# Kernel tuning notes

Hardware: AMD Instinct MI355X
Metric: run time of the kernel (lower is better)

## Reference

```python
import jax, jax.numpy as jnp
import numpy as np

N, IN_SIZE, FEAT, N_OUT = 8192, 512, 128, 512
ALPHA = 0.5


def setup_inputs() -> dict:
    key = jax.random.key(0)
    ks = jax.random.split(key, 5)
    return {
        "x": jax.random.normal(ks[0], (N, IN_SIZE), dtype=jnp.float32),
        "W0": jax.random.normal(ks[1], (FEAT, IN_SIZE), dtype=jnp.float32) * (1.0 / np.sqrt(IN_SIZE)),
        "W1": jax.random.normal(ks[2], (FEAT, IN_SIZE), dtype=jnp.float32) * (1.0 / np.sqrt(IN_SIZE)),
        "weight": jax.random.normal(ks[3], (IN_SIZE, N_OUT), dtype=jnp.float32),
        "weight_time": jax.random.normal(ks[4], (IN_SIZE, N_OUT), dtype=jnp.float32),
    }


def time_affinity(n: int) -> jnp.ndarray:
    # Closed form of the numpy roll/triu/flip construction: M[i,j] = n - |i-j|,
    # then rows normalized to sum to 1.
    idx = jnp.arange(n)
    M = (n - jnp.abs(idx[:, None] - idx[None, :])).astype(jnp.float32)
    return M / jnp.sum(M, axis=1, keepdims=True)


def reference(x, W0, W1, weight, weight_time):
    n = x.shape[0]
    q = x @ W0.T                      # [N, FEAT]
    k = x @ W1.T                      # [N, FEAT]
    G = jax.nn.softmax(q @ k.T, axis=1)   # [N, N] learned affinity
    G_time = time_affinity(n)              # [N, N] static affinity
    out = (G @ x) @ weight                 # [N, N_OUT]
    out_time = (G_time @ x) @ weight_time  # [N, N_OUT]
    return ALPHA * out + (1.0 - ALPHA) * out_time
```

## Files before the change

kernel.cpp:

```cpp
#include <hip/hip_runtime.h>
#include <math.h>

#define NN 8192
#define INS 512
#define FEAT 128

typedef unsigned short ush;
typedef short bf16x8 __attribute__((ext_vector_type(8)));
typedef float f32x4 __attribute__((ext_vector_type(4)));

__device__ __forceinline__ ush f2bf(float f) {
    unsigned u = __float_as_uint(f);
    unsigned r = (u + 0x7FFFu + ((u >> 16) & 1u)) >> 16;
    return (ush)r;
}
__device__ __forceinline__ float bf2f(ush h) {
    return __uint_as_float(((unsigned)h) << 16);
}
__device__ __forceinline__ void cp16(const ush* g, ush* l) {
    __builtin_amdgcn_global_load_lds(
        (const __attribute__((address_space(1))) void*)g,
        (__attribute__((address_space(3))) void*)l, 16, 0, 0);
}
__device__ __forceinline__ void split8(float4 f0, float4 f1, uint4& h, uint4& l) {
    float f[8] = {f0.x, f0.y, f0.z, f0.w, f1.x, f1.y, f1.z, f1.w};
    unsigned hu[8], lu[8];
    #pragma unroll
    for (int j = 0; j < 8; ++j) {
        unsigned u = __float_as_uint(f[j]);
        hu[j] = u >> 16;
        float lo = f[j] - __uint_as_float(u & 0xFFFF0000u);
        lu[j] = (unsigned)f2bf(lo);
    }
    h.x = hu[0] | (hu[1] << 16); h.y = hu[2] | (hu[3] << 16);
    h.z = hu[4] | (hu[5] << 16); h.w = hu[6] | (hu[7] << 16);
    l.x = lu[0] | (lu[1] << 16); l.y = lu[2] | (lu[3] << 16);
    l.z = lu[4] | (lu[5] << 16); l.w = lu[6] | (lu[7] << 16);
}


__global__ __launch_bounds__(256) void cast_w01(const float* __restrict__ W0,
                                                const float* __restrict__ W1,
                                                ush* __restrict__ W01h,
                                                ush* __restrict__ W01l) {
    int idx = (blockIdx.x * 256 + threadIdx.x) * 8;
    int r = idx >> 9, c = idx & 511;
    const float* src = (r < 128) ? &W0[r * 512 + c] : &W1[(r - 128) * 512 + c];
    float4 f0 = *(const float4*)src;
    float4 f1 = *(const float4*)(src + 4);
    uint4 h, l;
    split8(f0, f1, h, l);
    *(uint4*)&W01h[idx] = h;
    *(uint4*)&W01l[idx] = l;
}

__global__ __launch_bounds__(256) void cast_wT(const float* __restrict__ wm,
                                               const float* __restrict__ wt,
                                               ush* __restrict__ wmTh, ush* __restrict__ wmTl,
                                               ush* __restrict__ wtTh, ush* __restrict__ wtTl) {
    const float* src = blockIdx.z ? wt : wm;
    ush* oh = blockIdx.z ? wtTh : wmTh;
    ush* ol = blockIdx.z ? wtTl : wmTl;
    __shared__ float T[64][65];
    const int t = threadIdx.x;
    const int k0 = blockIdx.y * 64, n0 = blockIdx.x * 64;
    #pragma unroll
    for (int u = 0; u < 4; ++u) {
        int idx = u * 256 + t;
        int r = idx >> 4, c4 = (idx & 15) * 4;
        *(float4*)&T[r][c4] = *(const float4*)&src[(k0 + r) * 512 + n0 + c4];
    }
    __syncthreads();
    #pragma unroll
    for (int u = 0; u < 4; ++u) {
        int idx = u * 256 + t;
        int a = idx >> 4, b4 = (idx & 15) * 4;
        unsigned hu[4], lu[4];
        #pragma unroll
        for (int j = 0; j < 4; ++j) {
            float f = T[b4 + j][a];
            unsigned uu = __float_as_uint(f);
            hu[j] = uu >> 16;
            lu[j] = (unsigned)f2bf(f - __uint_as_float(uu & 0xFFFF0000u));
        }
        uint2 hp, lp;
        hp.x = hu[0] | (hu[1] << 16); hp.y = hu[2] | (hu[3] << 16);
        lp.x = lu[0] | (lu[1] << 16); lp.y = lu[2] | (lu[3] << 16);
        *(uint2*)&oh[(n0 + a) * 512 + k0 + b4] = hp;
        *(uint2*)&ol[(n0 + a) * 512 + k0 + b4] = lp;
    }
}

__global__ __launch_bounds__(256) void gemm_xv(const float* __restrict__ x,
    const ush* __restrict__ wmTh, const ush* __restrict__ wmTl,
    const ush* __restrict__ wtTh, const ush* __restrict__ wtTl,
    ush* __restrict__ vtg, ush* __restrict__ xtb) {
    const bool isV = (blockIdx.z == 0);
    const ush* Bhg = isV ? wmTh : wtTh;
    const ush* Blg = isV ? wmTl : wtTl;
    __shared__ __align__(16) ush sm[20480];
    ush* Ah = sm;
    ush* Al = sm + 5120;
    ush* Bh = sm + 10240;
    ush* Bl = sm + 15360;
    const int t = threadIdx.x;
    const int lane = t & 63, w = t >> 6;
    const int l15 = lane & 15, g4 = lane >> 4;
    const int m0 = blockIdx.y * 128, n0 = blockIdx.x * 128;
    const int wm0 = (w & 1) * 64, wn0 = (w >> 1) * 64;
    f32x4 acc[4][4];
    #pragma unroll
    for (int mt = 0; mt < 4; ++mt)
        #pragma unroll
        for (int nt = 0; nt < 4; ++nt)
            acc[mt][nt] = (f32x4){0.f, 0.f, 0.f, 0.f};

    const int am = t >> 1, akh = (t & 1) * 16;
    for (int k0 = 0; k0 < 512; k0 += 32) {
        __syncthreads();
        {
            const float* src = &x[(m0 + am) * 512 + k0 + akh];
            float4 f0 = *(const float4*)&src[0];
            float4 f1 = *(const float4*)&src[4];
            float4 f2 = *(const float4*)&src[8];
            float4 f3 = *(const float4*)&src[12];
            uint4 h0, l0, h1, l1;
            split8(f0, f1, h0, l0);
            split8(f2, f3, h1, l1);
            int s0 = am * 5 + (akh >> 3);
            *(uint4*)&Ah[s0 * 8] = h0; *(uint4*)&Ah[(s0 + 1) * 8] = h1;
            *(uint4*)&Al[s0 * 8] = l0; *(uint4*)&Al[(s0 + 1) * 8] = l1;
        }
        #pragma unroll
        for (int u = 0; u < 2; ++u) {
            int s = u * 256 + t;
            int n = s >> 2, g = s & 3;
            int srco = (n0 + n) * 512 + k0 + g * 8;
            int slot = n * 5 + g;
            *(uint4*)&Bh[slot * 8] = *(const uint4*)&Bhg[srco];
            *(uint4*)&Bl[slot * 8] = *(const uint4*)&Blg[srco];
        }
        __syncthreads();
        bf16x8 ah[4], al[4], bh[4], bl[4];
        #pragma unroll
        for (int mt = 0; mt < 4; ++mt) {
            int slot = (wm0 + mt * 16 + l15) * 5 + g4;
            ah[mt] = *(const bf16x8*)&Ah[slot * 8];
            al[mt] = *(const bf16x8*)&Al[slot * 8];
        }
        #pragma unroll
        for (int nt = 0; nt < 4; ++nt) {
            int slot = (wn0 + nt * 16 + l15) * 5 + g4;
            bh[nt] = *(const bf16x8*)&Bh[slot * 8];
            bl[nt] = *(const bf16x8*)&Bl[slot * 8];
        }
        #pragma unroll
        for (int mt = 0; mt < 4; ++mt)
            #pragma unroll
            for (int nt = 0; nt < 4; ++nt) {
                acc[mt][nt] = __builtin_amdgcn_mfma_f32_16x16x32_bf16(ah[mt], bh[nt], acc[mt][nt], 0, 0, 0);
                acc[mt][nt] = __builtin_amdgcn_mfma_f32_16x16x32_bf16(al[mt], bh[nt], acc[mt][nt], 0, 0, 0);
                acc[mt][nt] = __builtin_amdgcn_mfma_f32_16x16x32_bf16(ah[mt], bl[nt], acc[mt][nt], 0, 0, 0);
            }
    }

    if (!isV) {
        #pragma unroll
        for (int mt = 0; mt < 4; ++mt)
            #pragma unroll
            for (int nt = 0; nt < 4; ++nt) {
                int col = n0 + wn0 + nt * 16 + l15;
                int rowb = m0 + wm0 + mt * 16 + g4 * 4;
                #pragma unroll
                for (int reg = 0; reg < 4; ++reg)
                    xtb[(rowb + reg) * 512 + col] = f2bf(acc[mt][nt][reg]);
            }
    } else {
        __syncthreads();
        #pragma unroll
        for (int mt = 0; mt < 4; ++mt)
            #pragma unroll
            for (int nt = 0; nt < 4; ++nt) {
                int nl = wn0 + nt * 16 + l15;
                int mb = wm0 + mt * 16 + g4 * 4;
                uint2 pk;
                pk.x = (unsigned)f2bf(acc[mt][nt][0]) | ((unsigned)f2bf(acc[mt][nt][1]) << 16);
                pk.y = (unsigned)f2bf(acc[mt][nt][2]) | ((unsigned)f2bf(acc[mt][nt][3]) << 16);
                *(uint2*)&sm[nl * 136 + mb] = pk;
            }
        __syncthreads();
        int a = t >> 1, off = (t & 1) * 64;
        #pragma unroll
        for (int u = 0; u < 8; ++u)
            *(uint4*)&vtg[(n0 + a) * 8192 + m0 + off + u * 8] =
                *(const uint4*)&sm[a * 136 + off + u * 8];
    }
}

__global__ __launch_bounds__(256) void gemm_qk(const float* __restrict__ x,
    const ush* __restrict__ W01h, const ush* __restrict__ W01l,
    ush* __restrict__ qh, ush* __restrict__ ql,
    ush* __restrict__ kh, ush* __restrict__ kl) {
    __shared__ __align__(16) ush sm[15360];
    ush* Ah = sm;
    ush* Al = sm + 2560;
    ush* Bh = sm + 5120;
    ush* Bl = sm + 10240;
    const int t = threadIdx.x;
    const int lane = t & 63, w = t >> 6;
    const int l15 = lane & 15, g4 = lane >> 4;
    const int m0 = blockIdx.y * 64, n0 = blockIdx.x * 128;
    const int wm0 = (w & 1) * 32, wn0 = (w >> 1) * 64;
    f32x4 acc[2][4];
    #pragma unroll
    for (int mt = 0; mt < 2; ++mt)
        #pragma unroll
        for (int nt = 0; nt < 4; ++nt)
            acc[mt][nt] = (f32x4){0.f, 0.f, 0.f, 0.f};

    const int ar = t >> 2, ag = t & 3;
    for (int k0 = 0; k0 < 512; k0 += 32) {
        __syncthreads();
        {
            const float* src = &x[(m0 + ar) * 512 + k0 + ag * 8];
            float4 f0 = *(const float4*)&src[0];
            float4 f1 = *(const float4*)&src[4];
            uint4 h, l;
            split8(f0, f1, h, l);
            int slot = ar * 5 + ag;
            *(uint4*)&Ah[slot * 8] = h;
            *(uint4*)&Al[slot * 8] = l;
        }
        #pragma unroll
        for (int u = 0; u < 2; ++u) {
            int s = u * 256 + t;
            int n = s >> 2, g = s & 3;
            int srco = (n0 + n) * 512 + k0 + g * 8;
            int slot = n * 5 + g;
            *(uint4*)&Bh[slot * 8] = *(const uint4*)&W01h[srco];
            *(uint4*)&Bl[slot * 8] = *(const uint4*)&W01l[srco];
        }
        __syncthreads();
        bf16x8 ah[2], al[2], bh[4], bl[4];
        #pragma unroll
        for (int mt = 0; mt < 2; ++mt) {
            int slot = (wm0 + mt * 16 + l15) * 5 + g4;
            ah[mt] = *(const bf16x8*)&Ah[slot * 8];
            al[mt] = *(const bf16x8*)&Al[slot * 8];
        }
        #pragma unroll
        for (int nt = 0; nt < 4; ++nt) {
            int slot = (wn0 + nt * 16 + l15) * 5 + g4;
            bh[nt] = *(const bf16x8*)&Bh[slot * 8];
            bl[nt] = *(const bf16x8*)&Bl[slot * 8];
        }
        #pragma unroll
        for (int mt = 0; mt < 2; ++mt)
            #pragma unroll
            for (int nt = 0; nt < 4; ++nt) {
                acc[mt][nt] = __builtin_amdgcn_mfma_f32_16x16x32_bf16(ah[mt], bh[nt], acc[mt][nt], 0, 0, 0);
                acc[mt][nt] = __builtin_amdgcn_mfma_f32_16x16x32_bf16(al[mt], bh[nt], acc[mt][nt], 0, 0, 0);
                acc[mt][nt] = __builtin_amdgcn_mfma_f32_16x16x32_bf16(ah[mt], bl[nt], acc[mt][nt], 0, 0, 0);
            }
    }
    ush* oh = (n0 == 0) ? qh : kh;
    ush* ol = (n0 == 0) ? ql : kl;
    #pragma unroll
    for (int mt = 0; mt < 2; ++mt)
        #pragma unroll
        for (int nt = 0; nt < 4; ++nt) {
            int col = wn0 + nt * 16 + l15;
            int rowb = m0 + wm0 + mt * 16 + g4 * 4;
            #pragma unroll
            for (int reg = 0; reg < 4; ++reg) {
                float v = acc[mt][nt][reg];
                unsigned u = __float_as_uint(v);
                ush h = (ush)(u >> 16);
                ush lo = f2bf(v - __uint_as_float(u & 0xFFFF0000u));
                oh[(rowb + reg) * 128 + col] = h;
                ol[(rowb + reg) * 128 + col] = lo;
            }
        }
}

__global__ __launch_bounds__(256) void time_part1(const ush* __restrict__ xtb,
                                                  float* __restrict__ pP,
                                                  float* __restrict__ pQ) {
    int d = blockIdx.x * 256 + threadIdx.x;
    int r0 = blockIdx.y * 128;
    float sp = 0.f, sq = 0.f;
    for (int r = 0; r < 128; ++r) {
        float v = bf2f(xtb[(r0 + r) * 512 + d]);
        sp += v;
        sq += (float)(r0 + r) * v;
    }
    pP[blockIdx.y * 512 + d] = sp;
    pQ[blockIdx.y * 512 + d] = sq;
}

__global__ __launch_bounds__(512) void time_part2(float* __restrict__ pP,
                                                  float* __restrict__ pQ,
                                                  float* __restrict__ Ad,
                                                  float* __restrict__ Qt) {
    int d = threadIdx.x;
    float rp = 0.f, rq = 0.f;
    for (int c = 0; c < 64; ++c) {
        int idx = c * 512 + d;
        float p = pP[idx], qv = pQ[idx];
        pP[idx] = rp; pQ[idx] = rq;
        rp += p; rq += qv;
    }
    Ad[d] = rp; Qt[d] = rq;
}

__global__ __launch_bounds__(256) void time_part3(const ush* __restrict__ xtb,
                                                  const float* __restrict__ pP,
                                                  const float* __restrict__ pQ,
                                                  const float* __restrict__ Ad,
                                                  const float* __restrict__ Qt,
                                                  float* __restrict__ out) {
    int d = blockIdx.x * 256 + threadIdx.x;
    int r0 = blockIdx.y * 128;
    float P = pP[blockIdx.y * 512 + d];
    float Q = pQ[blockIdx.y * 512 + d];
    float A = Ad[d], Qtot = Qt[d];
    for (int r = 0; r < 128; ++r) {
        int i = r0 + r;
        float v = bf2f(xtb[i * 512 + d]);
        P += v;
        float fi = (float)i;
        Q += fi * v;
        float B = 2.f * fi * P - 2.f * Q + Qtot - fi * A;
        int Si = 67108864 - (i * (i + 1)) / 2 - ((8191 - i) * (8192 - i)) / 2;
        float T = (8192.f * A - B) / (float)Si;
        out[i * 512 + d] = 0.5f * T;
    }
}

__global__ __launch_bounds__(256, 2) void pass1(const ush* __restrict__ qhg,
                                                const ush* __restrict__ qlg,
                                                const ush* __restrict__ khg,
                                                const ush* __restrict__ klg,
                                                float* __restrict__ pm,
                                                float* __restrict__ pl) {
    __shared__ __align__(16) ush Kh3[3][32 * 128];
    __shared__ __align__(16) ush Kl3[3][32 * 128];
    __shared__ float sm_[2][128], sl_[2][128];
    const int t = threadIdx.x;
    const int lane = t & 63, w = t >> 6;
    const int rt0 = w & 1, ct = w >> 1;
    const int b = blockIdx.x;
    const int jc = b & 7, ib = b >> 3;
    const int i0 = ib * 128;
    const int jbase = jc * 1024;
    const int l15 = lane & 15, g = lane >> 4;

    bf16x8 Qh[4][4], Ql[4][4];
    #pragma unroll
    for (int rr = 0; rr < 4; ++rr) {
        int qrow = i0 + (rt0 + 2 * rr) * 16 + l15;
        #pragma unroll
        for (int kt = 0; kt < 4; ++kt) {
            Qh[rr][kt] = *(const bf16x8*)&qhg[qrow * 128 + kt * 32 + g * 8];
            Ql[rr][kt] = *(const bf16x8*)&qlg[qrow * 128 + kt * 32 + g * 8];
        }
    }
    float m_run[4][4], l_run[4][4];
    #pragma unroll
    for (int rr = 0; rr < 4; ++rr)
        #pragma unroll
        for (int reg = 0; reg < 4; ++reg) { m_run[rr][reg] = -INFINITY; l_run[rr][reg] = 0.f; }

    auto stageK = [&](ush* KhD, ush* KlD, int j0) {
        #pragma unroll
        for (int u = 0; u < 2; ++u) {
            int s = u * 256 + t;
            int n = s >> 4, gl = (s & 15) ^ (n & 15);
            int src = (j0 + n) * 128 + gl * 8;
            cp16(&khg[src], &KhD[s * 8]);
            cp16(&klg[src], &KlD[s * 8]);
        }
    };

    ush* KhC = Kh3[0]; ush* KlC = Kl3[0];
    ush* KhN = Kh3[1]; ush* KlN = Kl3[1];
    ush* KhP = Kh3[2]; ush* KlP = Kl3[2];

    stageK(KhC, KlC, jbase);
    stageK(KhN, KlN, jbase + 32);
    __syncthreads();

    for (int jt = 0; jt < 32; ++jt) {
        if (jt < 30) stageK(KhP, KlP, jbase + (jt + 2) * 32);

        bf16x8 kbh[4], kbl[4];
        {
            int n = ct * 16 + l15;
            #pragma unroll
            for (int kt = 0; kt < 4; ++kt) {
                int slot = n * 16 + ((kt * 4 + g) ^ (n & 15));
                kbh[kt] = *(const bf16x8*)&KhC[slot * 8];
                kbl[kt] = *(const bf16x8*)&KlC[slot * 8];
            }
        }
        #pragma unroll
        for (int rr = 0; rr < 4; ++rr) {
            f32x4 sa = {0.f, 0.f, 0.f, 0.f};
            f32x4 sb = {0.f, 0.f, 0.f, 0.f};
            f32x4 sc = {0.f, 0.f, 0.f, 0.f};
            #pragma unroll
            for (int kt = 0; kt < 4; ++kt) sa = __builtin_amdgcn_mfma_f32_16x16x32_bf16(Qh[rr][kt], kbh[kt], sa, 0, 0, 0);
            #pragma unroll
            for (int kt = 0; kt < 4; ++kt) sb = __builtin_amdgcn_mfma_f32_16x16x32_bf16(Ql[rr][kt], kbh[kt], sb, 0, 0, 0);
            #pragma unroll
            for (int kt = 0; kt < 4; ++kt) sc = __builtin_amdgcn_mfma_f32_16x16x32_bf16(Qh[rr][kt], kbl[kt], sc, 0, 0, 0);
            #pragma unroll
            for (int reg = 0; reg < 4; ++reg) {
                float s = (sa[reg] + sb[reg]) + sc[reg];
                float mn = fmaxf(m_run[rr][reg], s);
                l_run[rr][reg] = l_run[rr][reg] * __expf(m_run[rr][reg] - mn) + __expf(s - mn);
                m_run[rr][reg] = mn;
            }
        }

        __syncthreads();
        ush* th = KhC; KhC = KhN; KhN = KhP; KhP = th;
        ush* tl = KlC; KlC = KlN; KlN = KlP; KlP = tl;
    }
    #pragma unroll
    for (int st = 1; st < 16; st <<= 1) {
        #pragma unroll
        for (int rr = 0; rr < 4; ++rr)
            #pragma unroll
            for (int reg = 0; reg < 4; ++reg) {
                float mo = __shfl_xor(m_run[rr][reg], st);
                float lo = __shfl_xor(l_run[rr][reg], st);
                float mn = fmaxf(m_run[rr][reg], mo);
                l_run[rr][reg] = l_run[rr][reg] * __expf(m_run[rr][reg] - mn) + lo * __expf(mo - mn);
                m_run[rr][reg] = mn;
            }
    }
    if (l15 == 0) {
        #pragma unroll
        for (int rr = 0; rr < 4; ++rr)
            #pragma unroll
            for (int reg = 0; reg < 4; ++reg) {
                int row = (rt0 + 2 * rr) * 16 + g * 4 + reg;
                sm_[ct][row] = m_run[rr][reg];
                sl_[ct][row] = l_run[rr][reg];
            }
    }
    __syncthreads();
    if (t < 128) {
        float M = fmaxf(sm_[0][t], sm_[1][t]);
        float l = sl_[0][t] * __expf(sm_[0][t] - M) + sl_[1][t] * __expf(sm_[1][t] - M);
        pm[jc * 8192 + i0 + t] = M;
        pl[jc * 8192 + i0 + t] = l;
    }
}

__global__ __launch_bounds__(256) void merge_stats(const float* __restrict__ pm,
                                                   const float* __restrict__ pl,
                                                   float* __restrict__ Mrow,
                                                   float* __restrict__ Rl) {
    int i = blockIdx.x * 256 + threadIdx.x;
    float M = pm[i];
    #pragma unroll
    for (int js = 1; js < 8; ++js) M = fmaxf(M, pm[js * 8192 + i]);
    float l = 0.f;
    #pragma unroll
    for (int js = 0; js < 8; ++js) l += pl[js * 8192 + i] * __expf(pm[js * 8192 + i] - M);
    Mrow[i] = M;
    Rl[i] = 1.0f / l;
}

__global__ __launch_bounds__(512, 2) void pass2(const ush* __restrict__ qhg,
                                                const ush* __restrict__ qlg,
                                                const ush* __restrict__ khg,
                                                const ush* __restrict__ klg,
                                                const ush* __restrict__ vtg,
                                                const float* __restrict__ Mrow,
                                                const float* __restrict__ Rl,
                                                ush* __restrict__ part0,
                                                ush* __restrict__ part1) {
    __shared__ __align__(16) ush Kh0[512 * 8],  Kh1[512 * 8];
    __shared__ __align__(16) ush Kl0[512 * 8],  Kl1[512 * 8];
    __shared__ __align__(16) ush Vt0[2048 * 8], Vt1[2048 * 8];
    __shared__ __align__(16) ush Pd0[64 * 40],  Pd1[64 * 40];

    const int t = threadIdx.x;
    const int lane = t & 63, w = t >> 6;
    const int l15 = lane & 15, g = lane >> 4;
    const int b = blockIdx.x;
    const int xcd = b & 7, lid = b >> 3;
    const int jhalf = xcd >> 2;
    const int strip = (xcd & 3) * 32 + lid;
    const int i0 = strip * 64;
    const int jbase = jhalf * 4096;
    const bool isS = (w < 4);
    const int wp = w & 3;

    bf16x8 Qh[4], Ql[4];
    float Mv[4], Rv[4];
    if (isS) {
        int qrow = i0 + wp * 16 + l15;
        #pragma unroll
        for (int kt = 0; kt < 4; ++kt) {
            Qh[kt] = *(const bf16x8*)&qhg[qrow * 128 + kt * 32 + g * 8];
            Ql[kt] = *(const bf16x8*)&qlg[qrow * 128 + kt * 32 + g * 8];
        }
        #pragma unroll
        for (int reg = 0; reg < 4; ++reg) {
            int row = i0 + wp * 16 + g * 4 + reg;
            Mv[reg] = Mrow[row];
            Rv[reg] = Rl[row];
        }
    }

    f32x4 acc[8][4];
    #pragma unroll
    for (int mt = 0; mt < 8; ++mt)
        #pragma unroll
        for (int nt = 0; nt < 4; ++nt)
            acc[mt][nt] = (f32x4){0.f, 0.f, 0.f, 0.f};

    auto stageK = [&](ush* KhD, ush* KlD, int j0) {
        int n = t >> 4, gl = (t & 15) ^ (n & 15);
        int src = (j0 + n) * 128 + gl * 8;
        cp16(&khg[src], &KhD[t * 8]);
        cp16(&klg[src], &KlD[t * 8]);
    };
    auto stageV = [&](ush* VtD, int j0) {
        #pragma unroll
        for (int u = 0; u < 4; ++u) {
            int s = u * 512 + t;
            int c = s >> 2, gl = (s & 3) ^ ((c >> 1) & 3);
            cp16(&vtg[c * 8192 + j0 + gl * 8], &VtD[s * 8]);
        }
    };
    auto pvStep = [&](const ush* VtR, const ush* Pr) {
        bf16x8 Pb[4];
        #pragma unroll
        for (int nt = 0; nt < 4; ++nt)
            Pb[nt] = *(const bf16x8*)&Pr[(nt * 16 + l15) * 40 + g * 8];
        #pragma unroll
        for (int mt = 0; mt < 8; ++mt) {
            int c = wp * 128 + mt * 16 + l15;
            int slot = c * 4 + (g ^ ((c >> 1) & 3));
            bf16x8 vfr = *(const bf16x8*)&VtR[slot * 8];
            #pragma unroll
            for (int nt = 0; nt < 4; ++nt)
                acc[mt][nt] = __builtin_amdgcn_mfma_f32_16x16x32_bf16(vfr, Pb[nt], acc[mt][nt], 0, 0, 0);
        }
    };

    stageK(Kh0, Kl0, jbase);
    __syncthreads();

    for (int jt = 0; jt < 128; ++jt) {
        ush* KhC = (jt & 1) ? Kh1 : Kh0;
        ush* KlC = (jt & 1) ? Kl1 : Kl0;
        ush* KhN = (jt & 1) ? Kh0 : Kh1;
        ush* KlN = (jt & 1) ? Kl0 : Kl1;
        ush* VtW = (jt & 1) ? Vt1 : Vt0;
        ush* VtR = (jt & 1) ? Vt0 : Vt1;
        ush* Pw  = (jt & 1) ? Pd1 : Pd0;
        ush* Pr  = (jt & 1) ? Pd0 : Pd1;

        stageV(VtW, jbase + jt * 32);
        if (jt < 127) stageK(KhN, KlN, jbase + (jt + 1) * 32);

        if (isS) {
            #pragma unroll
            for (int kh = 0; kh < 2; ++kh) {
                bf16x8 kbh[4], kbl[4];
                int n = kh * 16 + l15;
                #pragma unroll
                for (int kt = 0; kt < 4; ++kt) {
                    int slot = n * 16 + ((kt * 4 + g) ^ (n & 15));
                    kbh[kt] = *(const bf16x8*)&KhC[slot * 8];
                    kbl[kt] = *(const bf16x8*)&KlC[slot * 8];
                }
                f32x4 sa = {0.f, 0.f, 0.f, 0.f};
                f32x4 sb = {0.f, 0.f, 0.f, 0.f};
                f32x4 sc = {0.f, 0.f, 0.f, 0.f};
                #pragma unroll
                for (int kt = 0; kt < 4; ++kt) sa = __builtin_amdgcn_mfma_f32_16x16x32_bf16(Qh[kt], kbh[kt], sa, 0, 0, 0);
                #pragma unroll
                for (int kt = 0; kt < 4; ++kt) sb = __builtin_amdgcn_mfma_f32_16x16x32_bf16(Ql[kt], kbh[kt], sb, 0, 0, 0);
                #pragma unroll
                for (int kt = 0; kt < 4; ++kt) sc = __builtin_amdgcn_mfma_f32_16x16x32_bf16(Qh[kt], kbl[kt], sc, 0, 0, 0);
                #pragma unroll
                for (int reg = 0; reg < 4; ++reg) {
                    float s = (sa[reg] + sb[reg]) + sc[reg];
                    float p = __expf(s - Mv[reg]) * Rv[reg];
                    Pw[(wp * 16 + g * 4 + reg) * 40 + kh * 16 + l15] = f2bf(p);
                }
            }
        } else if (jt > 0) {
            pvStep(VtR, Pr);
        }
        __syncthreads();
    }

    if (!isS) {
        pvStep(Vt1, Pd1);

        ush* prt = (jhalf == 0) ? part0 : part1;
        #pragma unroll
        for (int mt = 0; mt < 8; ++mt)
            #pragma unroll
            for (int nt = 0; nt < 4; ++nt) {
                int qrow = i0 + nt * 16 + l15;
                int vcol = wp * 128 + mt * 16 + g * 4;
                uint2 pk;
                pk.x = (unsigned)f2bf(acc[mt][nt][0]) | ((unsigned)f2bf(acc[mt][nt][1]) << 16);
                pk.y = (unsigned)f2bf(acc[mt][nt][2]) | ((unsigned)f2bf(acc[mt][nt][3]) << 16);
                *(uint2*)&prt[qrow * 512 + vcol] = pk;
            }
    }
}

__global__ __launch_bounds__(256) void merge_k(const ush* __restrict__ p0,
                                               const ush* __restrict__ p1,
                                               float* __restrict__ out) {
    int base = (blockIdx.x * 256 + threadIdx.x) * 8;
    uint4 a = *(const uint4*)&p0[base];
    uint4 b = *(const uint4*)&p1[base];
    float4 o0 = *(float4*)&out[base];
    float4 o1 = *(float4*)&out[base + 4];
    unsigned av[4] = {a.x, a.y, a.z, a.w};
    unsigned bv[4] = {b.x, b.y, b.z, b.w};
    float r[8];
    #pragma unroll
    for (int i = 0; i < 4; ++i) {
        r[2 * i + 0] = 0.5f * (bf2f((ush)(av[i] & 0xFFFF)) + bf2f((ush)(bv[i] & 0xFFFF)));
        r[2 * i + 1] = 0.5f * (bf2f((ush)(av[i] >> 16)) + bf2f((ush)(bv[i] >> 16)));
    }
    o0.x += r[0]; o0.y += r[1]; o0.z += r[2]; o0.w += r[3];
    o1.x += r[4]; o1.y += r[5]; o1.z += r[6]; o1.w += r[7];
    *(float4*)&out[base] = o0;
    *(float4*)&out[base + 4] = o1;
}

extern "C" void kernel_launch(void* const* d_in, const int* in_sizes, int n_in,
                              void* d_out, int out_size, void* d_ws, size_t ws_size,
                              hipStream_t stream) {
    const float* x  = (const float*)d_in[0];
    const float* W0 = (const float*)d_in[1];
    const float* W1 = (const float*)d_in[2];
    const float* wm = (const float*)d_in[3];
    const float* wt = (const float*)d_in[4];
    float* out = (float*)d_out;
    float* ws  = (float*)d_ws;

    ush* vtg = (ush*)(ws + 0);
    ush* xtb  = (ush*)(ws + 2097152);
    float* Mr = ws + 2097152;
    float* Rl = ws + 2105344;
    float* pm = ws + 2113536;
    float* pl = ws + 2179072;
    ush* W01h = (ush*)(ws + 4194304);
    ush* W01l = (ush*)(ws + 4259840);
    ush* wmTh = (ush*)(ws + 4325376);
    ush* wmTl = (ush*)(ws + 4456448);
    ush* wtTh = (ush*)(ws + 4587520);
    ush* wtTl = (ush*)(ws + 4718592);
    ush* part0 = (ush*)(ws + 4194304);
    ush* part1 = (ush*)(ws + 6291456);
    ush* qh = (ush*)(ws + 8388608);
    ush* ql = (ush*)(ws + 8912896);
    ush* kh = (ush*)(ws + 9437184);
    ush* kl = (ush*)(ws + 9961472);
    float* pP = ws + 10485760;
    float* pQ = ws + 10518528;
    float* Ad = ws + 10551296;
    float* Qt = ws + 10551808;

    cast_w01   <<<dim3(64),       256, 0, stream>>>(W0, W1, W01h, W01l);
    cast_wT    <<<dim3(8, 8, 2),  256, 0, stream>>>(wm, wt, wmTh, wmTl, wtTh, wtTl);
    gemm_xv    <<<dim3(4, 64, 2), 256, 0, stream>>>(x, wmTh, wmTl, wtTh, wtTl, vtg, xtb);
    gemm_qk    <<<dim3(2, 128),   256, 0, stream>>>(x, W01h, W01l, qh, ql, kh, kl);
    time_part1 <<<dim3(2, 64),    256, 0, stream>>>(xtb, pP, pQ);
    time_part2 <<<dim3(1),        512, 0, stream>>>(pP, pQ, Ad, Qt);
    time_part3 <<<dim3(2, 64),    256, 0, stream>>>(xtb, pP, pQ, Ad, Qt, out);
    pass1      <<<dim3(512),      256, 0, stream>>>(qh, ql, kh, kl, pm, pl);
    merge_stats<<<dim3(32),       256, 0, stream>>>(pm, pl, Mr, Rl);
    pass2      <<<dim3(256),      512, 0, stream>>>(qh, ql, kh, kl, vtg, Mr, Rl, part0, part1);
    merge_k    <<<dim3(2048),     256, 0, stream>>>(part0, part1, out);
}
```

Measured before the change: 374.4 us.

## Replace two-pass softmax with online softmax rescaling inside attention pass

Removes the separate row max/sum-exp pass (pass1) and merge_stats kernel, and computes running max and sum inside pass2 flash-attention style. Each row tile's rescale factor goes through shared memory so the PV warps can rescale their accumulators, skipping the rescale when every factor is 1. The two j-halves are combined in merge_k using their saved (m, l) statistics. This saves recomputing QK^T a second time, at the cost of extra shuffles, exps and accumulator rescales in the main loop.

```diff
diff --git a/kernel.cpp b/kernel.cpp
--- a/kernel.cpp
+++ b/kernel.cpp
@@ -337,156 +337,20 @@
     }
 }
 
-__global__ __launch_bounds__(256, 2) void pass1(const ush* __restrict__ qhg,
-                                                const ush* __restrict__ qlg,
-                                                const ush* __restrict__ khg,
-                                                const ush* __restrict__ klg,
-                                                float* __restrict__ pm,
-                                                float* __restrict__ pl) {
-    __shared__ __align__(16) ush Kh3[3][32 * 128];
-    __shared__ __align__(16) ush Kl3[3][32 * 128];
-    __shared__ float sm_[2][128], sl_[2][128];
-    const int t = threadIdx.x;
-    const int lane = t & 63, w = t >> 6;
-    const int rt0 = w & 1, ct = w >> 1;
-    const int b = blockIdx.x;
-    const int jc = b & 7, ib = b >> 3;
-    const int i0 = ib * 128;
-    const int jbase = jc * 1024;
-    const int l15 = lane & 15, g = lane >> 4;
-
-    bf16x8 Qh[4][4], Ql[4][4];
-    #pragma unroll
-    for (int rr = 0; rr < 4; ++rr) {
-        int qrow = i0 + (rt0 + 2 * rr) * 16 + l15;
-        #pragma unroll
-        for (int kt = 0; kt < 4; ++kt) {
-            Qh[rr][kt] = *(const bf16x8*)&qhg[qrow * 128 + kt * 32 + g * 8];
-            Ql[rr][kt] = *(const bf16x8*)&qlg[qrow * 128 + kt * 32 + g * 8];
-        }
-    }
-    float m_run[4][4], l_run[4][4];
-    #pragma unroll
-    for (int rr = 0; rr < 4; ++rr)
-        #pragma unroll
-        for (int reg = 0; reg < 4; ++reg) { m_run[rr][reg] = -INFINITY; l_run[rr][reg] = 0.f; }
-
-    auto stageK = [&](ush* KhD, ush* KlD, int j0) {
-        #pragma unroll
-        for (int u = 0; u < 2; ++u) {
-            int s = u * 256 + t;
-            int n = s >> 4, gl = (s & 15) ^ (n & 15);
-            int src = (j0 + n) * 128 + gl * 8;
-            cp16(&khg[src], &KhD[s * 8]);
-            cp16(&klg[src], &KlD[s * 8]);
-        }
-    };
-
-    ush* KhC = Kh3[0]; ush* KlC = Kl3[0];
-    ush* KhN = Kh3[1]; ush* KlN = Kl3[1];
-    ush* KhP = Kh3[2]; ush* KlP = Kl3[2];
-
-    stageK(KhC, KlC, jbase);
-    stageK(KhN, KlN, jbase + 32);
-    __syncthreads();
-
-    for (int jt = 0; jt < 32; ++jt) {
-        if (jt < 30) stageK(KhP, KlP, jbase + (jt + 2) * 32);
-
-        bf16x8 kbh[4], kbl[4];
-        {
-            int n = ct * 16 + l15;
-            #pragma unroll
-            for (int kt = 0; kt < 4; ++kt) {
-                int slot = n * 16 + ((kt * 4 + g) ^ (n & 15));
-                kbh[kt] = *(const bf16x8*)&KhC[slot * 8];
-                kbl[kt] = *(const bf16x8*)&KlC[slot * 8];
-            }
-        }
-        #pragma unroll
-        for (int rr = 0; rr < 4; ++rr) {
-            f32x4 sa = {0.f, 0.f, 0.f, 0.f};
-            f32x4 sb = {0.f, 0.f, 0.f, 0.f};
-            f32x4 sc = {0.f, 0.f, 0.f, 0.f};
-            #pragma unroll
-            for (int kt = 0; kt < 4; ++kt) sa = __builtin_amdgcn_mfma_f32_16x16x32_bf16(Qh[rr][kt], kbh[kt], sa, 0, 0, 0);
-            #pragma unroll
-            for (int kt = 0; kt < 4; ++kt) sb = __builtin_amdgcn_mfma_f32_16x16x32_bf16(Ql[rr][kt], kbh[kt], sb, 0, 0, 0);
-            #pragma unroll
-            for (int kt = 0; kt < 4; ++kt) sc = __builtin_amdgcn_mfma_f32_16x16x32_bf16(Qh[rr][kt], kbl[kt], sc, 0, 0, 0);
-            #pragma unroll
-            for (int reg = 0; reg < 4; ++reg) {
-                float s = (sa[reg] + sb[reg]) + sc[reg];
-                float mn = fmaxf(m_run[rr][reg], s);
-                l_run[rr][reg] = l_run[rr][reg] * __expf(m_run[rr][reg] - mn) + __expf(s - mn);
-                m_run[rr][reg] = mn;
-            }
-        }
-
-        __syncthreads();
-        ush* th = KhC; KhC = KhN; KhN = KhP; KhP = th;
-        ush* tl = KlC; KlC = KlN; KlN = KlP; KlP = tl;
-    }
-    #pragma unroll
-    for (int st = 1; st < 16; st <<= 1) {
-        #pragma unroll
-        for (int rr = 0; rr < 4; ++rr)
-            #pragma unroll
-            for (int reg = 0; reg < 4; ++reg) {
-                float mo = __shfl_xor(m_run[rr][reg], st);
-                float lo = __shfl_xor(l_run[rr][reg], st);
-                float mn = fmaxf(m_run[rr][reg], mo);
-                l_run[rr][reg] = l_run[rr][reg] * __expf(m_run[rr][reg] - mn) + lo * __expf(mo - mn);
-                m_run[rr][reg] = mn;
-            }
-    }
-    if (l15 == 0) {
-        #pragma unroll
-        for (int rr = 0; rr < 4; ++rr)
-            #pragma unroll
-            for (int reg = 0; reg < 4; ++reg) {
-                int row = (rt0 + 2 * rr) * 16 + g * 4 + reg;
-                sm_[ct][row] = m_run[rr][reg];
-                sl_[ct][row] = l_run[rr][reg];
-            }
-    }
-    __syncthreads();
-    if (t < 128) {
-        float M = fmaxf(sm_[0][t], sm_[1][t]);
-        float l = sl_[0][t] * __expf(sm_[0][t] - M) + sl_[1][t] * __expf(sm_[1][t] - M);
-        pm[jc * 8192 + i0 + t] = M;
-        pl[jc * 8192 + i0 + t] = l;
-    }
-}
-
-__global__ __launch_bounds__(256) void merge_stats(const float* __restrict__ pm,
-                                                   const float* __restrict__ pl,
-                                                   float* __restrict__ Mrow,
-                                                   float* __restrict__ Rl) {
-    int i = blockIdx.x * 256 + threadIdx.x;
-    float M = pm[i];
-    #pragma unroll
-    for (int js = 1; js < 8; ++js) M = fmaxf(M, pm[js * 8192 + i]);
-    float l = 0.f;
-    #pragma unroll
-    for (int js = 0; js < 8; ++js) l += pl[js * 8192 + i] * __expf(pm[js * 8192 + i] - M);
-    Mrow[i] = M;
-    Rl[i] = 1.0f / l;
-}
-
 __global__ __launch_bounds__(512, 2) void pass2(const ush* __restrict__ qhg,
                                                 const ush* __restrict__ qlg,
                                                 const ush* __restrict__ khg,
                                                 const ush* __restrict__ klg,
                                                 const ush* __restrict__ vtg,
-                                                const float* __restrict__ Mrow,
-                                                const float* __restrict__ Rl,
                                                 ush* __restrict__ part0,
-                                                ush* __restrict__ part1) {
+                                                ush* __restrict__ part1,
+                                                float* __restrict__ mh,
+                                                float* __restrict__ lh) {
     __shared__ __align__(16) ush Kh0[512 * 8],  Kh1[512 * 8];
     __shared__ __align__(16) ush Kl0[512 * 8],  Kl1[512 * 8];
     __shared__ __align__(16) ush Vt0[2048 * 8], Vt1[2048 * 8];
     __shared__ __align__(16) ush Pd0[64 * 40],  Pd1[64 * 40];
+    __shared__ float Sc0[64], Sc1[64], Linv[64];
 
     const int t = threadIdx.x;
     const int lane = t & 63, w = t >> 6;
@@ -501,7 +365,7 @@
     const int wp = w & 3;
 
     bf16x8 Qh[4], Ql[4];
-    float Mv[4], Rv[4];
+    float m_run[4], l_run[4];
     if (isS) {
         int qrow = i0 + wp * 16 + l15;
         #pragma unroll
@@ -510,11 +374,7 @@
             Ql[kt] = *(const bf16x8*)&qlg[qrow * 128 + kt * 32 + g * 8];
         }
         #pragma unroll
-        for (int reg = 0; reg < 4; ++reg) {
-            int row = i0 + wp * 16 + g * 4 + reg;
-            Mv[reg] = Mrow[row];
-            Rv[reg] = Rl[row];
-        }
+        for (int reg = 0; reg < 4; ++reg) { m_run[reg] = -INFINITY; l_run[reg] = 0.f; }
     }
 
     f32x4 acc[8][4];
@@ -538,7 +398,20 @@
             cp16(&vtg[c * 8192 + j0 + gl * 8], &VtD[s * 8]);
         }
     };
-    auto pvStep = [&](const ush* VtR, const ush* Pr) {
+    auto pvStep = [&](const ush* VtR, const ush* Pr, const float* Scr) {
+        float sc[4];
+        #pragma unroll
+        for (int nt = 0; nt < 4; ++nt) sc[nt] = Scr[nt * 16 + l15];
+        bool need = (sc[0] != 1.f) || (sc[1] != 1.f) || (sc[2] != 1.f) || (sc[3] != 1.f);
+        if (__any(need)) {
+            #pragma unroll
+            for (int mt = 0; mt < 8; ++mt)
+                #pragma unroll
+                for (int nt = 0; nt < 4; ++nt)
+                    #pragma unroll
+                    for (int reg = 0; reg < 4; ++reg)
+                        acc[mt][nt][reg] *= sc[nt];
+        }
         bf16x8 Pb[4];
         #pragma unroll
         for (int nt = 0; nt < 4; ++nt)
@@ -566,11 +439,14 @@
         ush* VtR = (jt & 1) ? Vt0 : Vt1;
         ush* Pw  = (jt & 1) ? Pd1 : Pd0;
         ush* Pr  = (jt & 1) ? Pd0 : Pd1;
+        float* Scw = (jt & 1) ? Sc1 : Sc0;
+        float* Scr = (jt & 1) ? Sc0 : Sc1;
 
         stageV(VtW, jbase + jt * 32);
         if (jt < 127) stageK(KhN, KlN, jbase + (jt + 1) * 32);
 
         if (isS) {
+            float sv[2][4];
             #pragma unroll
             for (int kh = 0; kh < 2; ++kh) {
                 bf16x8 kbh[4], kbl[4];
@@ -583,29 +459,59 @@
                 }
                 f32x4 sa = {0.f, 0.f, 0.f, 0.f};
                 f32x4 sb = {0.f, 0.f, 0.f, 0.f};
-                f32x4 sc = {0.f, 0.f, 0.f, 0.f};
+                f32x4 sc_ = {0.f, 0.f, 0.f, 0.f};
                 #pragma unroll
                 for (int kt = 0; kt < 4; ++kt) sa = __builtin_amdgcn_mfma_f32_16x16x32_bf16(Qh[kt], kbh[kt], sa, 0, 0, 0);
                 #pragma unroll
                 for (int kt = 0; kt < 4; ++kt) sb = __builtin_amdgcn_mfma_f32_16x16x32_bf16(Ql[kt], kbh[kt], sb, 0, 0, 0);
                 #pragma unroll
-                for (int kt = 0; kt < 4; ++kt) sc = __builtin_amdgcn_mfma_f32_16x16x32_bf16(Qh[kt], kbl[kt], sc, 0, 0, 0);
-                #pragma unroll
-                for (int reg = 0; reg < 4; ++reg) {
-                    float s = (sa[reg] + sb[reg]) + sc[reg];
-                    float p = __expf(s - Mv[reg]) * Rv[reg];
-                    Pw[(wp * 16 + g * 4 + reg) * 40 + kh * 16 + l15] = f2bf(p);
-                }
+                for (int kt = 0; kt < 4; ++kt) sc_ = __builtin_amdgcn_mfma_f32_16x16x32_bf16(Qh[kt], kbl[kt], sc_, 0, 0, 0);
+                #pragma unroll
+                for (int reg = 0; reg < 4; ++reg)
+                    sv[kh][reg] = (sa[reg] + sb[reg]) + sc_[reg];
+            }
+            #pragma unroll
+            for (int reg = 0; reg < 4; ++reg) {
+                float mx = fmaxf(sv[0][reg], sv[1][reg]);
+                #pragma unroll
+                for (int st = 1; st < 16; st <<= 1) mx = fmaxf(mx, __shfl_xor(mx, st));
+                float mn = fmaxf(m_run[reg], mx);
+                float scf = __expf(m_run[reg] - mn);
+                m_run[reg] = mn;
+                float p0 = __expf(sv[0][reg] - mn);
+                float p1 = __expf(sv[1][reg] - mn);
+                int row = wp * 16 + g * 4 + reg;
+                Pw[row * 40 + l15]      = f2bf(p0);
+                Pw[row * 40 + 16 + l15] = f2bf(p1);
+                float rs = p0 + p1;
+                #pragma unroll
+                for (int st = 1; st < 16; st <<= 1) rs += __shfl_xor(rs, st);
+                l_run[reg] = l_run[reg] * scf + rs;
+                if (l15 == 0) Scw[row] = scf;
             }
         } else if (jt > 0) {
-            pvStep(VtR, Pr);
+            pvStep(VtR, Pr, Scr);
         }
         __syncthreads();
     }
 
+    if (isS) {
+        #pragma unroll
+        for (int reg = 0; reg < 4; ++reg) {
+            int row = wp * 16 + g * 4 + reg;
+            if (l15 == 0) {
+                Linv[row] = 1.0f / l_run[reg];
+                mh[jhalf * 8192 + i0 + row] = m_run[reg];
+                lh[jhalf * 8192 + i0 + row] = l_run[reg];
+            }
+        }
+    }
+    __syncthreads();
     if (!isS) {
-        pvStep(Vt1, Pd1);
-
+        pvStep(Vt1, Pd1, Sc1);
+        float li[4];
+        #pragma unroll
+        for (int nt = 0; nt < 4; ++nt) li[nt] = Linv[nt * 16 + l15];
         ush* prt = (jhalf == 0) ? part0 : part1;
         #pragma unroll
         for (int mt = 0; mt < 8; ++mt)
@@ -614,8 +520,10 @@
                 int qrow = i0 + nt * 16 + l15;
                 int vcol = wp * 128 + mt * 16 + g * 4;
                 uint2 pk;
-                pk.x = (unsigned)f2bf(acc[mt][nt][0]) | ((unsigned)f2bf(acc[mt][nt][1]) << 16);
-                pk.y = (unsigned)f2bf(acc[mt][nt][2]) | ((unsigned)f2bf(acc[mt][nt][3]) << 16);
+                pk.x = (unsigned)f2bf(acc[mt][nt][0] * li[nt]) |
+                       ((unsigned)f2bf(acc[mt][nt][1] * li[nt]) << 16);
+                pk.y = (unsigned)f2bf(acc[mt][nt][2] * li[nt]) |
+                       ((unsigned)f2bf(acc[mt][nt][3] * li[nt]) << 16);
                 *(uint2*)&prt[qrow * 512 + vcol] = pk;
             }
     }
@@ -623,8 +531,18 @@
 
 __global__ __launch_bounds__(256) void merge_k(const ush* __restrict__ p0,
                                                const ush* __restrict__ p1,
+                                               const float* __restrict__ mh,
+                                               const float* __restrict__ lh,
                                                float* __restrict__ out) {
     int base = (blockIdx.x * 256 + threadIdx.x) * 8;
+    int row = base >> 9;
+    float m0 = mh[row], m1 = mh[8192 + row];
+    float l0 = lh[row], l1 = lh[8192 + row];
+    float M = fmaxf(m0, m1);
+    float w0 = l0 * __expf(m0 - M);
+    float w1 = l1 * __expf(m1 - M);
+    float z = 0.5f / (w0 + w1);
+    w0 *= z; w1 *= z;
     uint4 a = *(const uint4*)&p0[base];
     uint4 b = *(const uint4*)&p1[base];
     float4 o0 = *(float4*)&out[base];
@@ -634,8 +552,8 @@
     float r[8];
     #pragma unroll
     for (int i = 0; i < 4; ++i) {
-        r[2 * i + 0] = 0.5f * (bf2f((ush)(av[i] & 0xFFFF)) + bf2f((ush)(bv[i] & 0xFFFF)));
-        r[2 * i + 1] = 0.5f * (bf2f((ush)(av[i] >> 16)) + bf2f((ush)(bv[i] >> 16)));
+        r[2 * i + 0] = w0 * bf2f((ush)(av[i] & 0xFFFF)) + w1 * bf2f((ush)(bv[i] & 0xFFFF));
+        r[2 * i + 1] = w0 * bf2f((ush)(av[i] >> 16))    + w1 * bf2f((ush)(bv[i] >> 16));
     }
     o0.x += r[0]; o0.y += r[1]; o0.z += r[2]; o0.w += r[3];
     o1.x += r[4]; o1.y += r[5]; o1.z += r[6]; o1.w += r[7];
@@ -656,10 +574,8 @@
 
     ush* vtg = (ush*)(ws + 0);
     ush* xtb  = (ush*)(ws + 2097152);
-    float* Mr = ws + 2097152;
-    float* Rl = ws + 2105344;
-    float* pm = ws + 2113536;
-    float* pl = ws + 2179072;
+    float* mhp = ws + 2097152;
+    float* lhp = ws + 2113536;
     ush* W01h = (ush*)(ws + 4194304);
     ush* W01l = (ush*)(ws + 4259840);
     ush* wmTh = (ush*)(ws + 4325376);
@@ -684,8 +600,6 @@
     time_part1 <<<dim3(2, 64),    256, 0, stream>>>(xtb, pP, pQ);
     time_part2 <<<dim3(1),        512, 0, stream>>>(pP, pQ, Ad, Qt);
     time_part3 <<<dim3(2, 64),    256, 0, stream>>>(xtb, pP, pQ, Ad, Qt, out);
-    pass1      <<<dim3(512),      256, 0, stream>>>(qh, ql, kh, kl, pm, pl);
-    merge_stats<<<dim3(32),       256, 0, stream>>>(pm, pl, Mr, Rl);
-    pass2      <<<dim3(256),      512, 0, stream>>>(qh, ql, kh, kl, vtg, Mr, Rl, part0, part1);
-    merge_k    <<<dim3(2048),     256, 0, stream>>>(part0, part1, out);
-}
+    pass2      <<<dim3(256),      512, 0, stream>>>(qh, ql, kh, kl, vtg, part0, part1, mhp, lhp);
+    merge_k    <<<dim3(2048),     256, 0, stream>>>(part0, part1, mhp, lhp, out);
+}
```

After: 444.6 us. 18.8% more time.
